# Kernel tuning notes

Measured on AMD Instinct MI355X. Metric: run time of the kernel, lower is better.

## Reference

```python
import jax, jax.numpy as jnp
import numpy as np

NUM_REGIONS = 32   # region labels are 1..NUM_REGIONS, 0 = background
EPS = 1e-8


def setup_inputs() -> dict:
    key = jax.random.key(0)
    k1, k2 = jax.random.split(key)
    B, D, H, W = 4, 160, 192, 192
    x = jax.random.normal(k1, (B, 1, D, H, W), dtype=jnp.float32)
    # precomputed connected-component label map (0 = background)
    region_map = jax.random.randint(k2, (B, D, H, W), 0, NUM_REGIONS + 1, dtype=jnp.int32)
    return {"x": x, "region_map": region_map}


def _per_volume_sums(xf, seg):
    # xf: [V] sigmoid probs, seg: [V] region ids in [0, NUM_REGIONS]
    xs = jax.ops.segment_sum(xf, seg, num_segments=NUM_REGIONS + 1)
    cnt = jax.ops.segment_sum(jnp.ones_like(xf), seg, num_segments=NUM_REGIONS + 1)
    return xs, cnt


def reference(x, region_map):
    B = x.shape[0]
    probs = jax.nn.sigmoid(x)                      # x.dim()==5 -> sigmoid
    xf = probs.reshape(B, -1)                      # [B, V]
    seg = region_map.reshape(B, -1)                # [B, V]
    xs, cnt = jax.vmap(_per_volume_sums)(xf, seg)  # [B, R+1] each
    xs_r = xs[:, 1:]                               # per-region sum of sigmoid(x)
    cnt_r = cnt[:, 1:]                             # per-region voxel count (= sum of binary y)
    # dice over the region: y==1 inside the region, so intersection == xs_r
    dice = 2.0 * xs_r / (xs_r + cnt_r + EPS)       # [B, R]
    valid = cnt_r > 0                              # region actually present
    n_valid = jnp.sum(valid, axis=-1)              # [B]
    mean_dice = jnp.sum(jnp.where(valid, dice, 0.0), axis=-1) / jnp.maximum(n_valid, 1)
    loss_b = jnp.where(n_valid > 0, 1.0 - mean_dice, 1.0)  # num_features==0 -> loss 1.0
    return jnp.mean(loss_b)
```

## Files before the change

kernel.cpp:

```cpp
#include <hip/hip_runtime.h>

#define NUM_REGIONS 32
#define NBINS 33
#define BATCH 4
#define DHW (160*192*192)
#define NVEC_PER_BATCH (DHW/4)
#define BLOCKS_PER_BATCH 512
#define NBLOCKS (BATCH*BLOCKS_PER_BATCH)
#define VEC_PER_BLOCK (NVEC_PER_BATCH/BLOCKS_PER_BATCH)
#define ITERS 12
#define COL_STRIDE 129
#define QSCALE 262144.0f
#define INV_QSCALE (1.0f/262144.0f)
#define CNT_SHIFT 25
#define XS_MASK ((1u<<CNT_SHIFT)-1u)
#define EPS 1e-8f

__global__ __launch_bounds__(256) void region_sums_kernel(
    const float* __restrict__ x,
    const int*   __restrict__ seg,
    float*       __restrict__ ws)
{
    __shared__ unsigned int hist[NBINS * COL_STRIDE];
    __shared__ float part_xs [8][NBINS];
    __shared__ float part_cnt[8][NBINS];

    const int tid = threadIdx.x;
    const int col = tid >> 1;

    for (int i = tid; i < NBINS * COL_STRIDE; i += 256) hist[i] = 0u;
    __syncthreads();

    const int batch = blockIdx.x >> 9;
    const int local = blockIdx.x & 511;
    const int vbase = batch * NVEC_PER_BATCH + local * VEC_PER_BLOCK;

    const float4* __restrict__ xv4 = (const float4*)x;
    const int4*   __restrict__ sv4 = (const int4*)seg;

    #define OFFK(k) ((((k)*256 + tid) < VEC_PER_BLOCK) ? ((k)*256 + tid) : (VEC_PER_BLOCK-1))

    float4 xA = xv4[vbase + OFFK(0)]; int4 sA = sv4[vbase + OFFK(0)];
    float4 xB = xv4[vbase + OFFK(1)]; int4 sB = sv4[vbase + OFFK(1)];
    float4 xC = xv4[vbase + OFFK(2)]; int4 sC = sv4[vbase + OFFK(2)];

    #pragma unroll 1
    for (int k = 0; k < ITERS; ++k) {
        const int kn = (k + 3 < ITERS) ? (k + 3) : (ITERS - 1);
        float4 xN = xv4[vbase + OFFK(kn)];
        int4   sN = sv4[vbase + OFFK(kn)];

        float p0 = __fdividef(1.0f, 1.0f + __expf(-xA.x));
        float p1 = __fdividef(1.0f, 1.0f + __expf(-xA.y));
        float p2 = __fdividef(1.0f, 1.0f + __expf(-xA.z));
        float p3 = __fdividef(1.0f, 1.0f + __expf(-xA.w));

        unsigned q0 = (unsigned)(fmaf(p0, QSCALE, 0.5f)) + (1u << CNT_SHIFT);
        unsigned q1 = (unsigned)(fmaf(p1, QSCALE, 0.5f)) + (1u << CNT_SHIFT);
        unsigned q2 = (unsigned)(fmaf(p2, QSCALE, 0.5f)) + (1u << CNT_SHIFT);
        unsigned q3 = (unsigned)(fmaf(p3, QSCALE, 0.5f)) + (1u << CNT_SHIFT);

        if (k * 256 + tid < VEC_PER_BLOCK) {
            atomicAdd(&hist[sA.x * COL_STRIDE + col], q0);
            atomicAdd(&hist[sA.y * COL_STRIDE + col], q1);
            atomicAdd(&hist[sA.z * COL_STRIDE + col], q2);
            atomicAdd(&hist[sA.w * COL_STRIDE + col], q3);
        }

        xA = xB; sA = sB; xB = xC; sB = sC; xC = xN; sC = sN;
    }
    #undef OFFK
    __syncthreads();

    {
        const int bin = (tid & 31) + 1;
        const int g   = tid >> 5;
        float xs = 0.0f, cnt = 0.0f;
        #pragma unroll
        for (int j = 0; j < 16; ++j) {
            unsigned V = hist[bin * COL_STRIDE + g * 16 + j];
            cnt += (float)(V >> CNT_SHIFT);
            xs  += (float)(V & XS_MASK);
        }
        part_xs [g][bin] = xs;
        part_cnt[g][bin] = cnt;
    }
    __syncthreads();

    if (tid < 32) {
        const int bin = tid + 1;
        float xs = 0.0f, cnt = 0.0f;
        #pragma unroll
        for (int g = 0; g < 8; ++g) {
            xs  += part_xs [g][bin];
            cnt += part_cnt[g][bin];
        }
        atomicAdd(&ws[batch * NBINS + bin], xs * INV_QSCALE);
        atomicAdd(&ws[BATCH * NBINS + batch * NBINS + bin], cnt);
    }
}

__global__ void region_dice_final_kernel(
    const float* __restrict__ ws,
    float*       __restrict__ out)
{
    const int lane = threadIdx.x;
    float loss_sum = 0.0f;

    for (int b = 0; b < BATCH; ++b) {
        bool  valid = false;
        float dice  = 0.0f;
        if (lane >= 1 && lane <= NUM_REGIONS) {
            float xs  = ws[b * NBINS + lane];
            float cnt = ws[BATCH * NBINS + b * NBINS + lane];
            valid = (cnt > 0.0f);
            if (valid) dice = 2.0f * xs / (xs + cnt + EPS);
        }
        unsigned long long m = __ballot(valid);
        int n_valid = __popcll(m);

        float s = dice;
        #pragma unroll
        for (int off = 32; off >= 1; off >>= 1) s += __shfl_down(s, off);

        float mean_dice = s / (float)((n_valid > 1) ? n_valid : 1);
        float loss_b    = (n_valid > 0) ? (1.0f - mean_dice) : 1.0f;
        loss_sum += loss_b;
    }

    if (lane == 0) out[0] = loss_sum * (1.0f / BATCH);
}

extern "C" void kernel_launch(void* const* d_in, const int* in_sizes, int n_in,
                              void* d_out, int out_size, void* d_ws, size_t ws_size,
                              hipStream_t stream)
{
    const float* x   = (const float*)d_in[0];
    const int*   seg = (const int*)d_in[1];
    float*       ws  = (float*)d_ws;

    hipMemsetAsync(d_ws, 0, 2 * BATCH * NBINS * sizeof(float), stream);

    region_sums_kernel<<<NBLOCKS, 256, 0, stream>>>(x, seg, ws);
    region_dice_final_kernel<<<1, 64, 0, stream>>>(ws, (float*)d_out);
}
```

Baseline: 217.8 us.

## Split histogram work between LDS atomics and per-thread register accumulators

Part of each float4's voxels (x,y and z on even iterations) now go into 32 per-thread register accumulators via compare-select, with the count packed as +256 per hit into the float value. The remaining voxels still use packed LDS atomics. The register accumulators are reduced through shared memory at the end, and the kernel now declares a minimum of 4 blocks per SM. The aim is to cut LDS atomic contention, at the price of about 64 extra VALU ops per voxel, higher register pressure and a longer reduction tail; float precision in the packed accumulators may also drift.

```diff
diff --git a/kernel.cpp b/kernel.cpp
--- a/kernel.cpp
+++ b/kernel.cpp
@@ -10,20 +10,29 @@
 #define VEC_PER_BLOCK (NVEC_PER_BATCH/BLOCKS_PER_BATCH)
 #define ITERS 12
 #define COL_STRIDE 129
+#define RED_STRIDE 257
 #define QSCALE 262144.0f
 #define INV_QSCALE (1.0f/262144.0f)
 #define CNT_SHIFT 25
 #define XS_MASK ((1u<<CNT_SHIFT)-1u)
 #define EPS 1e-8f
 
-__global__ __launch_bounds__(256) void region_sums_kernel(
+__global__ __launch_bounds__(256, 4) void region_sums_kernel(
     const float* __restrict__ x,
     const int*   __restrict__ seg,
     float*       __restrict__ ws)
 {
     __shared__ unsigned int hist[NBINS * COL_STRIDE];
-    __shared__ float part_xs [8][NBINS];
-    __shared__ float part_cnt[8][NBINS];
+    __shared__ float part_h_xs [8][32];
+    __shared__ float part_h_cnt[8][32];
+    __shared__ float partA_xs[16][16];
+    __shared__ float partA_cnt[16][16];
+    __shared__ float tot_xs[32];
+    __shared__ float tot_cnt[32];
+
+    float acc[32];
+    #pragma unroll
+    for (int b = 0; b < 32; ++b) acc[b] = 0.0f;
 
     const int tid = threadIdx.x;
     const int col = tid >> 1;
@@ -55,16 +64,31 @@
         float p2 = __fdividef(1.0f, 1.0f + __expf(-xA.z));
         float p3 = __fdividef(1.0f, 1.0f + __expf(-xA.w));
 
-        unsigned q0 = (unsigned)(fmaf(p0, QSCALE, 0.5f)) + (1u << CNT_SHIFT);
-        unsigned q1 = (unsigned)(fmaf(p1, QSCALE, 0.5f)) + (1u << CNT_SHIFT);
-        unsigned q2 = (unsigned)(fmaf(p2, QSCALE, 0.5f)) + (1u << CNT_SHIFT);
-        unsigned q3 = (unsigned)(fmaf(p3, QSCALE, 0.5f)) + (1u << CNT_SHIFT);
-
-        if (k * 256 + tid < VEC_PER_BLOCK) {
-            atomicAdd(&hist[sA.x * COL_STRIDE + col], q0);
-            atomicAdd(&hist[sA.y * COL_STRIDE + col], q1);
-            atomicAdd(&hist[sA.z * COL_STRIDE + col], q2);
-            atomicAdd(&hist[sA.w * COL_STRIDE + col], q3);
+        const bool active = (k * 256 + tid) < VEC_PER_BLOCK;
+        if (active) {
+            unsigned qw = (unsigned)(fmaf(p3, QSCALE, 0.5f)) + (1u << CNT_SHIFT);
+            atomicAdd(&hist[sA.w * COL_STRIDE + col], qw);
+
+            float P0 = p0 + 256.0f;
+            float P1 = p1 + 256.0f;
+
+            if (k & 1) {
+                unsigned qz = (unsigned)(fmaf(p2, QSCALE, 0.5f)) + (1u << CNT_SHIFT);
+                atomicAdd(&hist[sA.z * COL_STRIDE + col], qz);
+                #pragma unroll
+                for (int b = 0; b < 32; ++b) {
+                    acc[b] += (sA.x == b + 1) ? P0 : 0.0f;
+                    acc[b] += (sA.y == b + 1) ? P1 : 0.0f;
+                }
+            } else {
+                float P2 = p2 + 256.0f;
+                #pragma unroll
+                for (int b = 0; b < 32; ++b) {
+                    acc[b] += (sA.x == b + 1) ? P0 : 0.0f;
+                    acc[b] += (sA.y == b + 1) ? P1 : 0.0f;
+                    acc[b] += (sA.z == b + 1) ? P2 : 0.0f;
+                }
+            }
         }
 
         xA = xB; sA = sB; xB = xC; sB = sC; xC = xN; sC = sN;
@@ -82,21 +106,69 @@
             cnt += (float)(V >> CNT_SHIFT);
             xs  += (float)(V & XS_MASK);
         }
-        part_xs [g][bin] = xs;
-        part_cnt[g][bin] = cnt;
+        part_h_xs [g][bin - 1] = xs * INV_QSCALE;
+        part_h_cnt[g][bin - 1] = cnt;
+    }
+    __syncthreads();
+
+    float* redf = (float*)hist;
+
+    #pragma unroll
+    for (int b = 0; b < 16; ++b) redf[b * RED_STRIDE + tid] = acc[b];
+    __syncthreads();
+    {
+        const int bin = tid & 15;
+        const int g   = tid >> 4;
+        float xs = 0.0f, cnt = 0.0f;
+        #pragma unroll
+        for (int j = 0; j < 16; ++j) {
+            float V = redf[bin * RED_STRIDE + g * 16 + j];
+            float c = truncf(V * (1.0f / 256.0f));
+            cnt += c;
+            xs  += V - 256.0f * c;
+        }
+        partA_xs [g][bin] = xs;
+        partA_cnt[g][bin] = cnt;
+    }
+    __syncthreads();
+    if (tid < 16) {
+        float xs = 0.0f, cnt = 0.0f;
+        #pragma unroll
+        for (int g = 0; g < 16; ++g) { xs += partA_xs[g][tid]; cnt += partA_cnt[g][tid]; }
+        tot_xs[tid] = xs; tot_cnt[tid] = cnt;
+    }
+    #pragma unroll
+    for (int b = 0; b < 16; ++b) redf[b * RED_STRIDE + tid] = acc[16 + b];
+    __syncthreads();
+    {
+        const int bin = tid & 15;
+        const int g   = tid >> 4;
+        float xs = 0.0f, cnt = 0.0f;
+        #pragma unroll
+        for (int j = 0; j < 16; ++j) {
+            float V = redf[bin * RED_STRIDE + g * 16 + j];
+            float c = truncf(V * (1.0f / 256.0f));
+            cnt += c;
+            xs  += V - 256.0f * c;
+        }
+        partA_xs [g][bin] = xs;
+        partA_cnt[g][bin] = cnt;
+    }
+    __syncthreads();
+    if (tid < 16) {
+        float xs = 0.0f, cnt = 0.0f;
+        #pragma unroll
+        for (int g = 0; g < 16; ++g) { xs += partA_xs[g][tid]; cnt += partA_cnt[g][tid]; }
+        tot_xs[16 + tid] = xs; tot_cnt[16 + tid] = cnt;
     }
     __syncthreads();
 
     if (tid < 32) {
-        const int bin = tid + 1;
-        float xs = 0.0f, cnt = 0.0f;
-        #pragma unroll
-        for (int g = 0; g < 8; ++g) {
-            xs  += part_xs [g][bin];
-            cnt += part_cnt[g][bin];
-        }
-        atomicAdd(&ws[batch * NBINS + bin], xs * INV_QSCALE);
-        atomicAdd(&ws[BATCH * NBINS + batch * NBINS + bin], cnt);
+        float xs = tot_xs[tid], cnt = tot_cnt[tid];
+        #pragma unroll
+        for (int g = 0; g < 8; ++g) { xs += part_h_xs[g][tid]; cnt += part_h_cnt[g][tid]; }
+        atomicAdd(&ws[batch * NBINS + tid + 1], xs);
+        atomicAdd(&ws[BATCH * NBINS + batch * NBINS + tid + 1], cnt);
     }
 }
 
```

Result: slower. 275.6 us (+26.5%).
